# Kernel tuning notes

Hardware: AMD Instinct MI355X
Metric: run time of the kernel (lower is better)

Reference implementation:

```python
import jax, jax.numpy as jnp
from jax import lax
import numpy as np

T, B, I, H = 2048, 64, 512, 512


def setup_inputs() -> dict:
    key = jax.random.key(0)
    k1, k2, k3 = jax.random.split(key, 3)
    # xavier-like scale for weights
    s_ih = float(np.sqrt(6.0 / (4 * H + I)))
    s_hh = float(np.sqrt(6.0 / (4 * H + H)))
    return {
        "word_seq": jax.random.normal(k1, (T, B, I), dtype=jnp.float32),
        "w_ih": jax.random.uniform(k2, (4 * H, I), dtype=jnp.float32, minval=-s_ih, maxval=s_ih),
        "w_hh": jax.random.uniform(k3, (4 * H, H), dtype=jnp.float32, minval=-s_hh, maxval=s_hh),
        "b_ih": jnp.zeros((4 * H,), dtype=jnp.float32),
        "b_hh": jnp.zeros((4 * H,), dtype=jnp.float32),
    }


def reference(word_seq, w_ih, w_hh, b_ih, b_hh):
    # word_seq: [T, B, I] (batch_first=False). Standard LSTM cell per step:
    # gates = x W_ih^T + b_ih + h W_hh^T + b_hh ; i,f,g,o split; c=f*c+i*g; h=o*tanh(c)
    Tn, Bn, _ = word_seq.shape
    Hn = w_hh.shape[1]
    # precompute input contribution for all timesteps (one big GEMM)
    x_gates = jnp.einsum("tbi,gi->tbg", word_seq, w_ih) + b_ih + b_hh  # [T, B, 4H]

    def step(carry, xg):
        h, c = carry
        gates = xg + h @ w_hh.T  # [B, 4H]
        i, f, g, o = jnp.split(gates, 4, axis=-1)
        i = jax.nn.sigmoid(i)
        f = jax.nn.sigmoid(f)
        g = jnp.tanh(g)
        o = jax.nn.sigmoid(o)
        c = f * c + i * g
        h = o * jnp.tanh(c)
        return (h, c), h

    h0 = jnp.zeros((Bn, Hn), dtype=word_seq.dtype)
    c0 = jnp.zeros((Bn, Hn), dtype=word_seq.dtype)
    (h, c), out = lax.scan(step, (h0, c0), x_gates)
    return out, (h, c)
```

## Files before the change

kernel.cpp:

```cpp
#include <hip/hip_runtime.h>
#include <hip/hip_bf16.h>
#include <stdint.h>


#define T_STEPS 2048
#define BATCH   64
#define IDIM    512
#define HDIM    512

typedef __attribute__((ext_vector_type(8))) short  vshort8;
typedef __attribute__((ext_vector_type(4))) float  vfloat4;

__device__ __forceinline__ unsigned short f2bf(float f) {
  unsigned int u = __builtin_bit_cast(unsigned int, f);
  u += 0x7fffu + ((u >> 16) & 1u);
  return (unsigned short)(u >> 16);
}

__device__ __forceinline__ vfloat4 mfma_bf16(vshort8 a, vshort8 b, vfloat4 c) {
  asm("v_mfma_f32_16x16x32_bf16 %0, %1, %2, %0" : "+v"(c) : "v"(a), "v"(b));
  return c;
}

__device__ __forceinline__ float sigmoid_(float x) {
  return 1.0f / (1.0f + __expf(-x));
}
__device__ __forceinline__ float tanh_(float x) {
  float ax = fabsf(x);
  float t  = __expf(-2.0f * ax);
  float y  = (1.0f - t) / (1.0f + t);
  return x < 0.0f ? -y : y;
}

__global__ void lstm_zero_ws(unsigned int* ws) {
  const int i = blockIdx.x * 256 + threadIdx.x;
  if (i < 34816) ws[i] = 0u;
}

__global__ __launch_bounds__(256, 1)
void lstm_persistent(const float* __restrict__ word_seq,
                     const float* __restrict__ w_ih,
                     const float* __restrict__ w_hh,
                     const float* __restrict__ b_ih,
                     const float* __restrict__ b_hh,
                     float* __restrict__ out,
                     unsigned int* __restrict__ flags,
                     unsigned short* __restrict__ hbuf) {
  __shared__ unsigned short x_s[32][520];
  __shared__ float red[4][2][4][16][20];

  const int tid  = threadIdx.x;
  const int blk  = blockIdx.x;
  const int bg   = blk >> 5;
  const int cg   = blk & 31;
  const int wv   = tid >> 6;
  const int lane = tid & 63;
  const int mrow = lane & 15;
  const int g4   = lane >> 4;

  vshort8 bw[2][4][4];
#pragma unroll
  for (int p = 0; p < 2; ++p) {
    const float* W = p ? w_hh : w_ih;
#pragma unroll
    for (int n = 0; n < 4; ++n) {
      const int gc = n * 512 + cg * 16 + mrow;
#pragma unroll
      for (int kk = 0; kk < 4; ++kk) {
        const int k0 = wv * 128 + kk * 32 + g4 * 8;
        const float* src = W + (size_t)gc * 512 + k0;
        vshort8 fr;
#pragma unroll
        for (int j = 0; j < 8; ++j) fr[j] = (short)f2bf(src[j]);
        bw[p][n][kk] = fr;
      }
    }
  }

  const int orow = tid >> 3;
  const int om   = (tid & 7) * 2;
  const int ort  = orow >> 4;
  const int odr  = orow & 15;

  float bsum[4][2];
#pragma unroll
  for (int n = 0; n < 4; ++n)
#pragma unroll
    for (int e = 0; e < 2; ++e) {
      const int gc = n * 512 + cg * 16 + om + e;
      bsum[n][e] = b_ih[gc] + b_hh[gc];
    }

  float cst[2]   = {0.0f, 0.0f};
  float hlast[2] = {0.0f, 0.0f};

#pragma unroll
  for (int it = 0; it < 16; ++it) {
    const int idx = it * 64 + lane;
    const int row = idx >> 5;
    const int c4  = idx & 31;
    const int col = wv * 128 + c4 * 4;
    const float4 v = *(const float4*)(word_seq + ((size_t)bg * 32 + row) * 512 + col);
    ushort4 us;
    us.x = f2bf(v.x); us.y = f2bf(v.y); us.z = f2bf(v.z); us.w = f2bf(v.w);
    *(ushort4*)&x_s[row][col] = us;
  }

  unsigned int* myflag = &flags[blk * 32];
  unsigned int* pollp  = &flags[(bg * 32 + (lane & 31)) * 32];

#pragma unroll 1
  for (int t = 0; t < T_STEPS; ++t) {
    vshort8 hfr[2][4];
    if (t > 0) {
      const unsigned short* hbR =
          hbuf + ((size_t)((t - 1) & 1) * BATCH + bg * 32) * 512;
#pragma unroll
      for (int r = 0; r < 2; ++r)
#pragma unroll
        for (int kk = 0; kk < 4; ++kk) {
          const int kb = wv * 128 + kk * 32 + g4 * 8;
          unsigned long long* p =
              (unsigned long long*)(hbR + (r * 16 + mrow) * 512 + kb);
          union { struct { unsigned long long lo, hi; } q; vshort8 v; } u;
          u.q.lo = __hip_atomic_load(p, __ATOMIC_RELAXED, __HIP_MEMORY_SCOPE_AGENT);
          u.q.hi = __hip_atomic_load(p + 1, __ATOMIC_RELAXED, __HIP_MEMORY_SCOPE_AGENT);
          hfr[r][kk] = u.v;
        }
    }

    vfloat4 acc[2][4];
#pragma unroll
    for (int r = 0; r < 2; ++r)
#pragma unroll
      for (int n = 0; n < 4; ++n) acc[r][n] = (vfloat4)0.0f;

#pragma unroll
    for (int kk = 0; kk < 4; ++kk) {
      const int kb = wv * 128 + kk * 32 + g4 * 8;
      const vshort8 a0 = *(const vshort8*)&x_s[mrow][kb];
      const vshort8 a1 = *(const vshort8*)&x_s[16 + mrow][kb];
#pragma unroll
      for (int n = 0; n < 4; ++n) {
        acc[0][n] = mfma_bf16(a0, bw[0][n][kk], acc[0][n]);
        acc[1][n] = mfma_bf16(a1, bw[0][n][kk], acc[1][n]);
      }
    }
    if (t > 0) {
#pragma unroll
      for (int kk = 0; kk < 4; ++kk)
#pragma unroll
        for (int n = 0; n < 4; ++n) {
          acc[0][n] = mfma_bf16(hfr[0][kk], bw[1][n][kk], acc[0][n]);
          acc[1][n] = mfma_bf16(hfr[1][kk], bw[1][n][kk], acc[1][n]);
        }
    }

    asm volatile("s_nop 7\n\ts_nop 7" ::: "memory");

#pragma unroll
    for (int r = 0; r < 2; ++r)
#pragma unroll
      for (int n = 0; n < 4; ++n)
        *(vfloat4*)&red[wv][r][n][mrow][g4 * 4] = acc[r][n];
    __syncthreads();

    float gate[4][2];
#pragma unroll
    for (int n = 0; n < 4; ++n) {
      float s0 = bsum[n][0], s1 = bsum[n][1];
#pragma unroll
      for (int w2 = 0; w2 < 4; ++w2) {
        s0 += red[w2][ort][n][om][odr];
        s1 += red[w2][ort][n][om + 1][odr];
      }
      gate[n][0] = s0; gate[n][1] = s1;
    }
    float hv[2];
#pragma unroll
    for (int e = 0; e < 2; ++e) {
      const float ig = sigmoid_(gate[0][e]);
      const float fg = sigmoid_(gate[1][e]);
      const float gg = tanh_(gate[2][e]);
      const float og = sigmoid_(gate[3][e]);
      cst[e] = fg * cst[e] + ig * gg;
      hv[e]  = og * tanh_(cst[e]);
    }
    hlast[0] = hv[0]; hlast[1] = hv[1];

    {
      float2 h2; h2.x = hv[0]; h2.y = hv[1];
      *(float2*)&out[((size_t)t * BATCH + bg * 32 + orow) * 512 + cg * 16 + om] = h2;
      const unsigned int packed =
          (unsigned int)f2bf(hv[0]) | ((unsigned int)f2bf(hv[1]) << 16);
      unsigned int* hbW = (unsigned int*)(hbuf +
          ((size_t)(t & 1) * BATCH + bg * 32) * 512 + orow * 512 + cg * 16 + om);
      __hip_atomic_store(hbW, packed, __ATOMIC_RELAXED, __HIP_MEMORY_SCOPE_AGENT);
    }

    asm volatile("s_waitcnt vmcnt(0)" ::: "memory");
    __syncthreads();
    if (tid == 0)
      __hip_atomic_fetch_add(myflag, 1u, __ATOMIC_RELAXED, __HIP_MEMORY_SCOPE_AGENT);

    if (t + 1 < T_STEPS) {
#pragma unroll
      for (int it = 0; it < 16; ++it) {
        const int idx = it * 64 + lane;
        const int row = idx >> 5;
        const int c4  = idx & 31;
        const int col = wv * 128 + c4 * 4;
        const float4 v = *(const float4*)(word_seq +
            ((size_t)(t + 1) * BATCH + bg * 32 + row) * 512 + col);
        ushort4 us;
        us.x = f2bf(v.x); us.y = f2bf(v.y); us.z = f2bf(v.z); us.w = f2bf(v.w);
        *(ushort4*)&x_s[row][col] = us;
      }
      {
        const unsigned int target = (unsigned int)(t + 1);
        int guard = 0;
        for (;;) {
          const unsigned int v = __hip_atomic_load(
              pollp, __ATOMIC_RELAXED, __HIP_MEMORY_SCOPE_AGENT);
          if (__ballot(v < target) == 0ull) break;
          if (++guard > (1 << 20)) break;
        }
      }
      asm volatile("" ::: "memory");
    }
  }

  {
    const size_t tail = (size_t)T_STEPS * BATCH * HDIM;
    const size_t gb   = (size_t)bg * 32 + orow;
    const int    col  = cg * 16 + om;
    float2 h2; h2.x = hlast[0]; h2.y = hlast[1];
    float2 c2; c2.x = cst[0];   c2.y = cst[1];
    *(float2*)&out[tail + gb * 512 + col] = h2;
    *(float2*)&out[tail + (size_t)BATCH * HDIM + gb * 512 + col] = c2;
  }
}

extern "C" void kernel_launch(void* const* d_in, const int* in_sizes, int n_in,
                              void* d_out, int out_size, void* d_ws, size_t ws_size,
                              hipStream_t stream) {
  (void)in_sizes; (void)n_in; (void)out_size; (void)ws_size;
  const float* word_seq = (const float*)d_in[0];
  const float* w_ih     = (const float*)d_in[1];
  const float* w_hh     = (const float*)d_in[2];
  const float* b_ih     = (const float*)d_in[3];
  const float* b_hh     = (const float*)d_in[4];
  float* out = (float*)d_out;

  unsigned int*   flags = (unsigned int*)d_ws;
  unsigned short* hbuf  = (unsigned short*)((char*)d_ws + 8192);

  lstm_zero_ws<<<136, 256, 0, stream>>>((unsigned int*)d_ws);
  lstm_persistent<<<64, 256, 0, stream>>>(word_seq, w_ih, w_hh, b_ih, b_hh,
                                          out, flags, hbuf);
}
```

Measured before the change: 20.83 ms.

## Replace flag-counter barrier with parity-tagged h values polled directly

Drops the per-block flag counters and the spin-wait on them. The exchanged bf16 h values now carry a generation parity in their low mantissa bit, and readers poll the h buffer itself until every word has the expected parity. The input-projection MFMAs are issued before the h poll so they overlap the wait, and the vmcnt drain plus flag atomic per step are gone. In exchange the low bit of each bf16 h is perturbed, which adds a small precision error, and correctness now depends on 32-bit store atomicity and the parity scheme.

New measurement: 21.73 ms. 1.04x slower.

```diff
diff --git a/kernel.cpp b/kernel.cpp
--- a/kernel.cpp
+++ b/kernel.cpp
@@ -44,7 +44,6 @@
                      const float* __restrict__ b_ih,
                      const float* __restrict__ b_hh,
                      float* __restrict__ out,
-                     unsigned int* __restrict__ flags,
                      unsigned short* __restrict__ hbuf) {
   __shared__ unsigned short x_s[32][520];
   __shared__ float red[4][2][4][16][20];
@@ -106,29 +105,8 @@
     *(ushort4*)&x_s[row][col] = us;
   }
 
-  unsigned int* myflag = &flags[blk * 32];
-  unsigned int* pollp  = &flags[(bg * 32 + (lane & 31)) * 32];
-
 #pragma unroll 1
   for (int t = 0; t < T_STEPS; ++t) {
-    vshort8 hfr[2][4];
-    if (t > 0) {
-      const unsigned short* hbR =
-          hbuf + ((size_t)((t - 1) & 1) * BATCH + bg * 32) * 512;
-#pragma unroll
-      for (int r = 0; r < 2; ++r)
-#pragma unroll
-        for (int kk = 0; kk < 4; ++kk) {
-          const int kb = wv * 128 + kk * 32 + g4 * 8;
-          unsigned long long* p =
-              (unsigned long long*)(hbR + (r * 16 + mrow) * 512 + kb);
-          union { struct { unsigned long long lo, hi; } q; vshort8 v; } u;
-          u.q.lo = __hip_atomic_load(p, __ATOMIC_RELAXED, __HIP_MEMORY_SCOPE_AGENT);
-          u.q.hi = __hip_atomic_load(p + 1, __ATOMIC_RELAXED, __HIP_MEMORY_SCOPE_AGENT);
-          hfr[r][kk] = u.v;
-        }
-    }
-
     vfloat4 acc[2][4];
 #pragma unroll
     for (int r = 0; r < 2; ++r)
@@ -146,7 +124,44 @@
         acc[1][n] = mfma_bf16(a1, bw[0][n][kk], acc[1][n]);
       }
     }
+
     if (t > 0) {
+      const unsigned gr = (((unsigned)(t - 1) >> 1) & 1u) ^ 1u;
+      const unsigned short* hbR =
+          hbuf + ((size_t)((t - 1) & 1) * BATCH + bg * 32) * 512;
+      vshort8 hfr[2][4];
+      unsigned bad = 1u;
+      int guard = 0;
+      while (__ballot(bad != 0u) != 0ull) {
+        if (bad) {
+          bad = 0u;
+#pragma unroll
+          for (int r = 0; r < 2; ++r)
+#pragma unroll
+            for (int kk = 0; kk < 4; ++kk) {
+              const int kb = wv * 128 + kk * 32 + g4 * 8;
+              const unsigned long long* p =
+                  (const unsigned long long*)(hbR + (r * 16 + mrow) * 512 + kb);
+              union { struct { unsigned long long lo, hi; } q; vshort8 v; } u;
+              u.q.lo = __hip_atomic_load(p,     __ATOMIC_RELAXED,
+                                         __HIP_MEMORY_SCOPE_AGENT);
+              u.q.hi = __hip_atomic_load(p + 1, __ATOMIC_RELAXED,
+                                         __HIP_MEMORY_SCOPE_AGENT);
+              hfr[r][kk] = u.v;
+              const unsigned w0 = (unsigned)u.q.lo;
+              const unsigned w1 = (unsigned)(u.q.lo >> 32);
+              const unsigned w2 = (unsigned)u.q.hi;
+              const unsigned w3 = (unsigned)(u.q.hi >> 32);
+              bad |= (((w0 ^ (w0 >> 16)) & 1u) | ((w0 & 1u) ^ gr));
+              bad |= (((w1 ^ (w1 >> 16)) & 1u) | ((w1 & 1u) ^ gr));
+              bad |= (((w2 ^ (w2 >> 16)) & 1u) | ((w2 & 1u) ^ gr));
+              bad |= (((w3 ^ (w3 >> 16)) & 1u) | ((w3 & 1u) ^ gr));
+            }
+        }
+        if (++guard > (1 << 14)) break;
+      }
+      asm volatile("" ::: "memory");
+
 #pragma unroll
       for (int kk = 0; kk < 4; ++kk)
 #pragma unroll
@@ -176,6 +191,8 @@
       }
       gate[n][0] = s0; gate[n][1] = s1;
     }
+    __syncthreads();
+
     float hv[2];
 #pragma unroll
     for (int e = 0; e < 2; ++e) {
@@ -189,19 +206,17 @@
     hlast[0] = hv[0]; hlast[1] = hv[1];
 
     {
-      float2 h2; h2.x = hv[0]; h2.y = hv[1];
-      *(float2*)&out[((size_t)t * BATCH + bg * 32 + orow) * 512 + cg * 16 + om] = h2;
-      const unsigned int packed =
-          (unsigned int)f2bf(hv[0]) | ((unsigned int)f2bf(hv[1]) << 16);
+      const unsigned gw = (((unsigned)t >> 1) & 1u) ^ 1u;
+      unsigned u0 = f2bf(hv[0]);  u0 += ((u0 & 1u) ^ gw);
+      unsigned u1 = f2bf(hv[1]);  u1 += ((u1 & 1u) ^ gw);
+      const unsigned packed = (u0 & 0xffffu) | (u1 << 16);
       unsigned int* hbW = (unsigned int*)(hbuf +
           ((size_t)(t & 1) * BATCH + bg * 32) * 512 + orow * 512 + cg * 16 + om);
       __hip_atomic_store(hbW, packed, __ATOMIC_RELAXED, __HIP_MEMORY_SCOPE_AGENT);
-    }
-
-    asm volatile("s_waitcnt vmcnt(0)" ::: "memory");
-    __syncthreads();
-    if (tid == 0)
-      __hip_atomic_fetch_add(myflag, 1u, __ATOMIC_RELAXED, __HIP_MEMORY_SCOPE_AGENT);
+
+      float2 h2; h2.x = hv[0]; h2.y = hv[1];
+      *(float2*)&out[((size_t)t * BATCH + bg * 32 + orow) * 512 + cg * 16 + om] = h2;
+    }
 
     if (t + 1 < T_STEPS) {
 #pragma unroll
@@ -216,17 +231,6 @@
         us.x = f2bf(v.x); us.y = f2bf(v.y); us.z = f2bf(v.z); us.w = f2bf(v.w);
         *(ushort4*)&x_s[row][col] = us;
       }
-      {
-        const unsigned int target = (unsigned int)(t + 1);
-        int guard = 0;
-        for (;;) {
-          const unsigned int v = __hip_atomic_load(
-              pollp, __ATOMIC_RELAXED, __HIP_MEMORY_SCOPE_AGENT);
-          if (__ballot(v < target) == 0ull) break;
-          if (++guard > (1 << 20)) break;
-        }
-      }
-      asm volatile("" ::: "memory");
     }
   }
 
@@ -252,10 +256,9 @@
   const float* b_hh     = (const float*)d_in[4];
   float* out = (float*)d_out;
 
-  unsigned int*   flags = (unsigned int*)d_ws;
-  unsigned short* hbuf  = (unsigned short*)((char*)d_ws + 8192);
+  unsigned short* hbuf = (unsigned short*)((char*)d_ws + 8192);
 
   lstm_zero_ws<<<136, 256, 0, stream>>>((unsigned int*)d_ws);
   lstm_persistent<<<64, 256, 0, stream>>>(word_seq, w_ih, w_hh, b_ih, b_hh,
-                                          out, flags, hbuf);
-}
+                                          out, hbuf);
+}
```
